# Optimization experiments

Hardware: AMD Instinct MI355X
Metric: run time of the kernel (lower is better)

## Reference

```python
import jax, jax.numpy as jnp
import numpy as np

B, N, F_IN = 8, 1024, 64
HEADS = 8
D = F_IN  # out_features per head (in_features == out_features)


def setup_inputs() -> dict:
    key = jax.random.key(0)
    ks = jax.random.split(key, 5)
    stdv = 1.0 / np.sqrt(F_IN * HEADS)
    h = jax.random.normal(ks[0], (B, N, F_IN), dtype=jnp.float32)
    adj = jnp.ones((B, N, N), dtype=jnp.float32)  # passed but unused by the module
    W = jax.random.uniform(ks[1], (F_IN, D * HEADS), minval=-stdv, maxval=stdv, dtype=jnp.float32)
    a = jax.random.uniform(ks[2], (2 * D, 1), minval=-stdv, maxval=stdv, dtype=jnp.float32)
    out_W = jax.random.normal(ks[3], (D * HEADS, F_IN), dtype=jnp.float32) / np.sqrt(D * HEADS)
    out_b = jnp.zeros((F_IN,), dtype=jnp.float32)
    return {"h": h, "adj": adj, "W": W, "a": a, "out_W": out_W, "out_b": out_b}


def reference(h, adj, W, a, out_W, out_b):
    Bv, Nv, _ = h.shape
    Dh = W.shape[1] // HEADS
    # Wh: [B, N, H, D]
    Wh = (h @ W).reshape(Bv, Nv, HEADS, Dh)
    # Additive attention decomposed: e[b,i,j,h] = leaky_relu(Wh[b,i,h].a_src + Wh[b,j,h].a_dst)
    a_src = jnp.einsum('bnhd,d->bnh', Wh, a[:Dh, 0])
    a_dst = jnp.einsum('bnhd,d->bnh', Wh, a[Dh:, 0])
    e = jax.nn.leaky_relu(a_src[:, :, None, :] + a_dst[:, None, :, :], negative_slope=0.01)  # [B,N,N,H]
    # Module applies softmax over dim=1 (the first node axis i)
    attn = jax.nn.softmax(e, axis=1)  # [B,N,N,H]
    # h_prime[b,i,h,:] = sum_j attn[b,i,j,h] * Wh[b,j,h,:]
    h_prime = jnp.einsum('bijh,bjhd->bihd', attn, Wh).reshape(Bv, Nv, HEADS * Dh)
    return h_prime @ out_W + out_b
```

## Files before the change

### kernel.cpp

```cpp
#include <hip/hip_runtime.h>


#define B_  8
#define N_  1024
#define H_  8
#define D_  64
#define BH_ 64

__device__ __forceinline__ float bcast_lane(float v, int l) {
  return __int_as_float(__builtin_amdgcn_readlane(__float_as_int(v), l));
}

__global__ __launch_bounds__(256) void k_wh(
    const float* __restrict__ h, const float* __restrict__ W,
    const float* __restrict__ a,
    float* __restrict__ Wh, float* __restrict__ sArr, float* __restrict__ tArr) {
  const int tid = threadIdx.x;
  const int lane = tid & 63;
  const int wid = tid >> 6;
  const int row0 = blockIdx.x * 16;
  const int b = row0 >> 10;

  float hreg[16];
#pragma unroll
  for (int r = 0; r < 16; ++r) hreg[r] = h[(row0 + r) * 64 + lane];
  const float a_s = a[lane];
  const float a_t = a[64 + lane];

  float acc0[16], acc1[16];
#pragma unroll
  for (int r = 0; r < 16; ++r) { acc0[r] = 0.f; acc1[r] = 0.f; }
#pragma unroll 4
  for (int k = 0; k < 64; ++k) {
    const float w0 = W[k * 512 + tid];
    const float w1 = W[k * 512 + tid + 256];
#pragma unroll
    for (int r = 0; r < 16; ++r) {
      const float hv = bcast_lane(hreg[r], k);
      acc0[r] += hv * w0;
      acc1[r] += hv * w1;
    }
  }
  const int hh0 = wid, hh1 = wid + 4;
#pragma unroll
  for (int r = 0; r < 16; ++r) {
    const int n = (row0 + r) & (N_ - 1);
    Wh[((b * H_ + hh0) * N_ + n) * D_ + lane] = acc0[r];
    Wh[((b * H_ + hh1) * N_ + n) * D_ + lane] = acc1[r];
  }
#pragma unroll
  for (int r = 0; r < 16; ++r) {
    const int n = (row0 + r) & (N_ - 1);
    float s0 = acc0[r] * a_s, t0 = acc0[r] * a_t;
    float s1 = acc1[r] * a_s, t1 = acc1[r] * a_t;
#pragma unroll
    for (int m = 32; m > 0; m >>= 1) {
      s0 += __shfl_xor(s0, m); t0 += __shfl_xor(t0, m);
      s1 += __shfl_xor(s1, m); t1 += __shfl_xor(t1, m);
    }
    if (lane == 0) {
      sArr[(b * H_ + hh0) * N_ + n] = s0;
      tArr[(b * H_ + hh0) * N_ + n] = t0;
      sArr[(b * H_ + hh1) * N_ + n] = s1;
      tArr[(b * H_ + hh1) * N_ + n] = t1;
    }
  }
}

__global__ __launch_bounds__(1024) void k_rest(
    const float* __restrict__ sArr, const float* __restrict__ tArr,
    const float* __restrict__ Wh,
    const float* __restrict__ outW, const float* __restrict__ outb,
    float* __restrict__ out) {
  __shared__ float2 uni[65 * 64];
  float* sL      = (float*)uni;
  float* tvL     = sL + 1024;
  float* cum1L   = tvL + 1024;
  float* cum001L = cum1L + 1024;
  float2* csOff  = uni;
  __shared__ int   tiL[1024];
  __shared__ float uL[1024], vL[1024];
  __shared__ int   rkL[1024];
  __shared__ float esL[1024], es001L[1024];
  __shared__ float ws1[16], ws2[16];

  const int tid = threadIdx.x;
  const int lane = tid & 63;
  const int wv = tid >> 6;
  const int bi = blockIdx.x;
  const int bh = bi & 63, q = bi >> 6;
  const int b = bh >> 3, hh = bh & 7;

  const float orig_s = sArr[bh * N_ + tid];
  float sv_r = orig_s;
  float tv_r = tArr[bh * N_ + tid];
  int   ti_r = tid;

  for (int size = 2; size <= 1024; size <<= 1) {
    for (int stride = size >> 1; stride > 0; stride >>= 1) {
      const bool up = ((tid & size) == 0);
      const bool lower = ((tid & stride) == 0);
      float psv, ptv; int pti;
      if (stride >= 64) {
        sL[tid] = sv_r; tvL[tid] = tv_r; tiL[tid] = ti_r;
        __syncthreads();
        const int p = tid ^ stride;
        psv = sL[p]; ptv = tvL[p]; pti = tiL[p];
        __syncthreads();
      } else {
        psv = __shfl_xor(sv_r, stride);
        ptv = __shfl_xor(tv_r, stride);
        pti = __shfl_xor(ti_r, stride);
      }
      const bool sameDir = (up == lower);
      const bool pLessS = (psv < sv_r);
      if (pLessS == sameDir) sv_r = psv;
      const bool pLessT = (ptv < tv_r) || (ptv == tv_r && pti < ti_r);
      if (pLessT == sameDir) { tv_r = ptv; ti_r = pti; }
    }
  }
  sL[tid] = sv_r; tvL[tid] = tv_r; tiL[tid] = ti_r;

  float c1 = __expf(sv_r), c001 = __expf(0.01f * sv_r);
  {
    float a1 = c1, a2 = c001;
#pragma unroll
    for (int off = 1; off < 64; off <<= 1) {
      const float x1 = __shfl_up(a1, off);
      const float x2 = __shfl_up(a2, off);
      if (lane >= off) { a1 += x1; a2 += x2; }
    }
    if (lane == 63) { ws1[wv] = a1; ws2[wv] = a2; }
    __syncthreads();
    float o1 = 0.f, o2 = 0.f;
    for (int ww = 0; ww < 16; ++ww) {
      if (ww < wv) { o1 += ws1[ww]; o2 += ws2[ww]; }
    }
    c1 = a1 + o1; c001 = a2 + o2;
  }
  cum1L[tid] = c1; cum001L[tid] = c001;
  __syncthreads();
  const float totalHi = cum1L[1023];

  float u_r, v_r;
  {
    const float tj = tv_r;
    const float th = -tj;
    int lo = 0, hi = 1024;
    while (lo < hi) { const int mid = (lo + hi) >> 1; if (sL[mid] <= th) lo = mid + 1; else hi = mid; }
    const float S_lo = (lo > 0) ? cum001L[lo - 1] : 0.f;
    const float S_hi = totalHi - ((lo > 0) ? cum1L[lo - 1] : 0.f);
    const float et = __expf(tj), et001 = __expf(0.01f * tj);
    const float Z = et * S_hi + et001 * S_lo;
    u_r = et / Z; v_r = et001 / Z;
    uL[tid] = u_r; vL[tid] = v_r;
  }
  {
    const float th = -orig_s;
    int lo = 0, hi = 1024;
    while (lo < hi) { const int mid = (lo + hi) >> 1; if (tvL[mid] <= th) lo = mid + 1; else hi = mid; }
    rkL[tid] = lo;
    esL[tid] = __expf(orig_s);
    es001L[tid] = __expf(0.01f * orig_s);
  }
  __syncthreads();

  const int whb = bh * (N_ * D_);
  {
    float r1 = 0.f, r2 = 0.f;
#pragma unroll 8
    for (int k2 = 0; k2 < 64; ++k2) {
      const int   j  = __builtin_amdgcn_readlane(ti_r, k2);
      const float uu = bcast_lane(u_r, k2);
      const float vv = bcast_lane(v_r, k2);
      const float w  = Wh[whb + j * 64 + lane];
      r1 += uu * w; r2 += vv * w;
      if ((k2 & 15) == 15) {
        csOff[(4 * wv + (k2 >> 4) + 1) * 64 + lane] = make_float2(r1, r2);
        r1 = 0.f; r2 = 0.f;
      }
    }
  }
  if (tid < 64) csOff[tid] = make_float2(0.f, 0.f);
  __syncthreads();

  float2 off[4];
  float2 tot = make_float2(0.f, 0.f);
  {
#pragma unroll
    for (int cc = 0; cc < 4; ++cc) {
      const int c = wv * 4 + cc;
      float o1 = 0.f, o2 = 0.f;
      for (int m = 1; m <= c; ++m) {
        const float2 cv = csOff[m * 64 + lane];
        o1 += cv.x; o2 += cv.y;
      }
      off[cc] = make_float2(o1, o2);
      if (c == 63) {
        const float2 last = csOff[64 * 64 + lane];
        tot = make_float2(o1 + last.x, o2 + last.y);
      }
    }
  }
  __syncthreads();
#pragma unroll
  for (int cc = 0; cc < 4; ++cc)
    csOff[(wv * 4 + cc) * 64 + lane] = off[cc];
  if (wv == 15) csOff[64 * 64 + lane] = tot;
  __syncthreads();

  const int rbase = q * 256 + wv * 16;
  const float T1 = csOff[64 * 64 + lane].x;
  float hpv[16];
#pragma unroll 2
  for (int r = 0; r < 16; ++r) {
    const int i = rbase + r;
    const int rk = rkL[i];
    float i1 = 0.f, i2 = 0.f;
    if (rk > 0) {
      const int idx = rk - 1, c = idx >> 4;
      const float2 co = csOff[c * 64 + lane];
      i1 = co.x; i2 = co.y;
      for (int k = c * 16; k <= idx; ++k) {
        const int j = tiL[k];
        const float w = Wh[whb + j * 64 + lane];
        i1 += uL[k] * w;
        i2 += vL[k] * w;
      }
    }
    hpv[r] = esL[i] * (T1 - i1) + es001L[i] * i2;
  }

  float acc[16];
  const float binit = (hh == 0) ? outb[lane] : 0.f;
#pragma unroll
  for (int r = 0; r < 16; ++r) acc[r] = binit;
#pragma unroll 4
  for (int kc = 0; kc < 64; ++kc) {
    const float wvv = outW[(hh * 64 + kc) * 64 + lane];
#pragma unroll
    for (int r = 0; r < 16; ++r) acc[r] += bcast_lane(hpv[r], kc) * wvv;
  }
#pragma unroll
  for (int r = 0; r < 16; ++r)
    atomicAdd(&out[(b * N_ + rbase + r) * 64 + lane], acc[r]);
}

extern "C" void kernel_launch(void* const* d_in, const int* in_sizes, int n_in,
                              void* d_out, int out_size, void* d_ws, size_t ws_size,
                              hipStream_t stream) {
  const float* h    = (const float*)d_in[0];
  const float* W    = (const float*)d_in[2];
  const float* a    = (const float*)d_in[3];
  const float* outW = (const float*)d_in[4];
  const float* outb = (const float*)d_in[5];
  float* out = (float*)d_out;

  float* ws   = (float*)d_ws;
  float* Wh   = ws;
  float* sArr = Wh + (size_t)BH_ * N_ * D_;
  float* tArr = sArr + BH_ * N_;

  hipMemsetAsync(out, 0, (size_t)B_ * N_ * 64 * sizeof(float), stream);
  hipLaunchKernelGGL(k_wh,   dim3((B_ * N_) / 16), dim3(256), 0, stream,
                     h, W, a, Wh, sArr, tArr);
  hipLaunchKernelGGL(k_rest, dim3(BH_ * 4), dim3(1024), 0, stream,
                     sArr, tArr, Wh, outW, outb, out);
}
```

Measured before the change: 178.4 us.

## Fold output bias init into k_wh and streamline prefix-sum and tail loops in k_rest

Removes the hipMemsetAsync on the output. Instead, k_wh writes the bias into the output buffer, so k_rest only accumulates with atomics. In k_rest, the chunk prefix offsets are now computed with a per-wave total scan, replacing the serial O(c) summation across chunks, which cuts one barrier. The tail loop per row becomes a fixed, fully unrolled 16-step loop that broadcasts indices and weights from registers via readlane and masks entries past the tail, rather than a variable-length loop reading from LDS. Exp factors are recomputed per lane instead of stored in shared memory, which saves LDS at the cost of more register pressure and wasted masked loads.

```diff
diff --git a/kernel.cpp b/kernel.cpp
--- a/kernel.cpp
+++ b/kernel.cpp
@@ -13,8 +13,9 @@
 
 __global__ __launch_bounds__(256) void k_wh(
     const float* __restrict__ h, const float* __restrict__ W,
-    const float* __restrict__ a,
-    float* __restrict__ Wh, float* __restrict__ sArr, float* __restrict__ tArr) {
+    const float* __restrict__ a, const float* __restrict__ outb,
+    float* __restrict__ Wh, float* __restrict__ sArr, float* __restrict__ tArr,
+    float* __restrict__ out) {
   const int tid = threadIdx.x;
   const int lane = tid & 63;
   const int wid = tid >> 6;
@@ -27,6 +28,10 @@
   const float a_s = a[lane];
   const float a_t = a[64 + lane];
 
+  const float bv = outb[tid & 63];
+#pragma unroll
+  for (int j = 0; j < 4; ++j) out[row0 * 64 + j * 256 + tid] = bv;
+
   float acc0[16], acc1[16];
 #pragma unroll
   for (int r = 0; r < 16; ++r) { acc0[r] = 0.f; acc1[r] = 0.f; }
@@ -70,7 +75,7 @@
 __global__ __launch_bounds__(1024) void k_rest(
     const float* __restrict__ sArr, const float* __restrict__ tArr,
     const float* __restrict__ Wh,
-    const float* __restrict__ outW, const float* __restrict__ outb,
+    const float* __restrict__ outW,
     float* __restrict__ out) {
   __shared__ float2 uni[65 * 64];
   float* sL      = (float*)uni;
@@ -78,11 +83,11 @@
   float* cum1L   = tvL + 1024;
   float* cum001L = cum1L + 1024;
   float2* csOff  = uni;
-  __shared__ int   tiL[1024];
-  __shared__ float uL[1024], vL[1024];
-  __shared__ int   rkL[1024];
-  __shared__ float esL[1024], es001L[1024];
-  __shared__ float ws1[16], ws2[16];
+  __shared__ int    tiL[1024];
+  __shared__ float2 uvL[1024];
+  __shared__ int    rkL[1024];
+  __shared__ float2 wsTL[16 * 64];
+  __shared__ float  ws1[16], ws2[16];
 
   const int tid = threadIdx.x;
   const int lane = tid & 63;
@@ -153,88 +158,82 @@
     const float et = __expf(tj), et001 = __expf(0.01f * tj);
     const float Z = et * S_hi + et001 * S_lo;
     u_r = et / Z; v_r = et001 / Z;
-    uL[tid] = u_r; vL[tid] = v_r;
+    uvL[tid] = make_float2(u_r, v_r);
   }
   {
     const float th = -orig_s;
     int lo = 0, hi = 1024;
     while (lo < hi) { const int mid = (lo + hi) >> 1; if (tvL[mid] <= th) lo = mid + 1; else hi = mid; }
     rkL[tid] = lo;
-    esL[tid] = __expf(orig_s);
-    es001L[tid] = __expf(0.01f * orig_s);
-  }
+  }
+
+  const int whb = bh * (N_ * D_);
+  float s1[4] = {0.f, 0.f, 0.f, 0.f}, s2[4] = {0.f, 0.f, 0.f, 0.f};
+#pragma unroll
+  for (int k2 = 0; k2 < 64; ++k2) {
+    const int   j  = __builtin_amdgcn_readlane(ti_r, k2);
+    const float uu = bcast_lane(u_r, k2);
+    const float vv = bcast_lane(v_r, k2);
+    const float w  = Wh[whb + j * 64 + lane];
+    s1[k2 >> 4] += uu * w;
+    s2[k2 >> 4] += vv * w;
+  }
+  wsTL[wv * 64 + lane] = make_float2(s1[0] + s1[1] + s1[2] + s1[3],
+                                     s2[0] + s2[1] + s2[2] + s2[3]);
   __syncthreads();
-
-  const int whb = bh * (N_ * D_);
-  {
-    float r1 = 0.f, r2 = 0.f;
-#pragma unroll 8
-    for (int k2 = 0; k2 < 64; ++k2) {
-      const int   j  = __builtin_amdgcn_readlane(ti_r, k2);
-      const float uu = bcast_lane(u_r, k2);
-      const float vv = bcast_lane(v_r, k2);
-      const float w  = Wh[whb + j * 64 + lane];
-      r1 += uu * w; r2 += vv * w;
-      if ((k2 & 15) == 15) {
-        csOff[(4 * wv + (k2 >> 4) + 1) * 64 + lane] = make_float2(r1, r2);
-        r1 = 0.f; r2 = 0.f;
-      }
-    }
-  }
-  if (tid < 64) csOff[tid] = make_float2(0.f, 0.f);
+  float o1 = 0.f, o2 = 0.f;
+  for (int ww = 0; ww < 16; ++ww) {
+    if (ww < wv) { const float2 t = wsTL[ww * 64 + lane]; o1 += t.x; o2 += t.y; }
+  }
+  {
+    float p1 = o1, p2 = o2;
+#pragma unroll
+    for (int cc = 0; cc < 4; ++cc) {
+      csOff[(4 * wv + cc) * 64 + lane] = make_float2(p1, p2);
+      p1 += s1[cc]; p2 += s2[cc];
+    }
+    if (wv == 15) csOff[64 * 64 + lane] = make_float2(p1, p2);
+  }
   __syncthreads();
 
-  float2 off[4];
-  float2 tot = make_float2(0.f, 0.f);
-  {
-#pragma unroll
-    for (int cc = 0; cc < 4; ++cc) {
-      const int c = wv * 4 + cc;
-      float o1 = 0.f, o2 = 0.f;
-      for (int m = 1; m <= c; ++m) {
-        const float2 cv = csOff[m * 64 + lane];
-        o1 += cv.x; o2 += cv.y;
-      }
-      off[cc] = make_float2(o1, o2);
-      if (c == 63) {
-        const float2 last = csOff[64 * 64 + lane];
-        tot = make_float2(o1 + last.x, o2 + last.y);
-      }
-    }
-  }
-  __syncthreads();
-#pragma unroll
-  for (int cc = 0; cc < 4; ++cc)
-    csOff[(wv * 4 + cc) * 64 + lane] = off[cc];
-  if (wv == 15) csOff[64 * 64 + lane] = tot;
-  __syncthreads();
-
   const int rbase = q * 256 + wv * 16;
+  const int rl = lane & 15;
+  const int   rk_p  = rkL[rbase + rl];
+  const float sq    = sArr[bh * N_ + rbase + rl];
+  const float es_p  = __expf(sq);
+  const float e01_p = __expf(0.01f * sq);
   const float T1 = csOff[64 * 64 + lane].x;
   float hpv[16];
-#pragma unroll 2
+#pragma unroll
   for (int r = 0; r < 16; ++r) {
-    const int i = rbase + r;
-    const int rk = rkL[i];
+    const int rk = __builtin_amdgcn_readlane(rk_p, r);
     float i1 = 0.f, i2 = 0.f;
     if (rk > 0) {
       const int idx = rk - 1, c = idx >> 4;
       const float2 co = csOff[c * 64 + lane];
       i1 = co.x; i2 = co.y;
-      for (int k = c * 16; k <= idx; ++k) {
-        const int j = tiL[k];
+      const int kb = c * 16;
+      const int    ti_p = tiL[kb + rl];
+      const float2 uv_p = uvL[kb + rl];
+      const int tail = idx & 15;
+#pragma unroll
+      for (int kk = 0; kk < 16; ++kk) {
+        const int j = __builtin_amdgcn_readlane(ti_p, kk);
+        float uu = bcast_lane(uv_p.x, kk);
+        float vv = bcast_lane(uv_p.y, kk);
+        uu = (kk <= tail) ? uu : 0.f;
+        vv = (kk <= tail) ? vv : 0.f;
         const float w = Wh[whb + j * 64 + lane];
-        i1 += uL[k] * w;
-        i2 += vL[k] * w;
+        i1 += uu * w;
+        i2 += vv * w;
       }
     }
-    hpv[r] = esL[i] * (T1 - i1) + es001L[i] * i2;
+    hpv[r] = bcast_lane(es_p, r) * (T1 - i1) + bcast_lane(e01_p, r) * i2;
   }
 
   float acc[16];
-  const float binit = (hh == 0) ? outb[lane] : 0.f;
-#pragma unroll
-  for (int r = 0; r < 16; ++r) acc[r] = binit;
+#pragma unroll
+  for (int r = 0; r < 16; ++r) acc[r] = 0.f;
 #pragma unroll 4
   for (int kc = 0; kc < 64; ++kc) {
     const float wvv = outW[(hh * 64 + kc) * 64 + lane];
@@ -261,9 +260,8 @@
   float* sArr = Wh + (size_t)BH_ * N_ * D_;
   float* tArr = sArr + BH_ * N_;
 
-  hipMemsetAsync(out, 0, (size_t)B_ * N_ * 64 * sizeof(float), stream);
   hipLaunchKernelGGL(k_wh,   dim3((B_ * N_) / 16), dim3(256), 0, stream,
-                     h, W, a, Wh, sArr, tArr);
+                     h, W, a, outb, Wh, sArr, tArr, out);
   hipLaunchKernelGGL(k_rest, dim3(BH_ * 4), dim3(1024), 0, stream,
-                     sArr, tArr, Wh, outW, outb, out);
-}
+                     sArr, tArr, Wh, outW, out);
+}
```

Result: faster. 172.1 us (-3.5%).
